# Optimization experiments

Hardware: AMD Instinct MI355X
Metric: run time of the kernel (lower is better)

## Reference

```python
import jax, jax.numpy as jnp
import numpy as np

NUM_STEPS = 50
NUM_DOF = 1
NVAR = NUM_STEPS * NUM_DOF
T = 0.05
V_MAX, A_MAX, J_MAX = 1.0, 2.0, 5.0
P_MAX = np.pi
THETA0 = 0.0
RHO = 1.0
MAXITER = 15
BATCH = 32768
HIDDEN = 1024
EPS = 1e-5


def _build_mats():
    # finite-difference operators (num_dof=1 so kron with eye(1) is identity)
    P_vel = np.eye(NUM_STEPS)
    P_acc = np.diff(P_vel, axis=0) / T          # (49, 50)
    P_jerk = np.diff(P_acc, axis=0) / T         # (48, 50)
    P_pos = np.cumsum(P_vel, axis=0) * T        # (50, 50)
    A_control = np.vstack([P_vel, -P_vel, P_acc, -P_acc,
                           P_jerk, -P_jerk, P_pos, -P_pos]).astype(np.float32)  # (394, 50)
    A_eq = np.zeros((2, NUM_STEPS), np.float32)
    A_eq[0, 0] = 1.0
    A_eq[1, -1] = 1.0
    cost = np.eye(NVAR) + RHO * A_control.T @ A_control
    Q = np.block([[cost, A_eq.T], [A_eq, np.zeros((2, 2))]])
    Q_inv = np.linalg.inv(Q).astype(np.float32)  # (52, 52)
    na = NUM_STEPS - 1
    nj = na - 1
    # limits used inside the iteration (p_max on both halves)
    b_iter = np.concatenate([np.full(2 * NUM_STEPS, V_MAX), np.full(2 * na, A_MAX),
                             np.full(2 * nj, J_MAX), np.full(2 * NUM_STEPS, P_MAX)]).astype(np.float32)
    # limits used for the slack init (p_max -/+ theta_init)
    b_init = np.concatenate([np.full(2 * NUM_STEPS, V_MAX), np.full(2 * na, A_MAX),
                             np.full(2 * nj, J_MAX), np.full(NUM_STEPS, P_MAX - THETA0),
                             np.full(NUM_STEPS, P_MAX + THETA0)]).astype(np.float32)
    return jnp.asarray(A_control), jnp.asarray(Q_inv), jnp.asarray(b_iter), jnp.asarray(b_init)


def _bn(x, g, b):
    # BatchNorm1d in training mode: biased batch statistics
    m = jnp.mean(x, axis=0)
    v = jnp.var(x, axis=0)
    return g * (x - m) * jax.lax.rsqrt(v + EPS) + b


def setup_inputs() -> dict:
    key = jax.random.key(0)
    ks = jax.random.split(key, 6)
    x = jax.random.normal(ks[0], (BATCH, NVAR), jnp.float32)
    W1 = jax.random.normal(ks[1], (NVAR, HIDDEN), jnp.float32) * 0.1
    W2 = jax.random.normal(ks[2], (HIDDEN, HIDDEN), jnp.float32) * 0.03
    W3 = jax.random.normal(ks[3], (HIDDEN, 256), jnp.float32) * 0.03
    W4 = jax.random.normal(ks[4], (256, 2 * NVAR), jnp.float32) * 0.06
    z = lambda n: jnp.zeros((n,), jnp.float32)
    o = lambda n: jnp.ones((n,), jnp.float32)
    return {"xi_samples_input_nn": x,
            "W1": W1, "b1": z(HIDDEN), "g1": o(HIDDEN), "be1": z(HIDDEN),
            "W2": W2, "b2": z(HIDDEN), "g2": o(HIDDEN), "be2": z(HIDDEN),
            "W3": W3, "b3": z(256), "g3": o(256), "be3": z(256),
            "W4": W4, "b4": z(2 * NVAR)}


def reference(xi_samples_input_nn, W1, b1, g1, be1, W2, b2, g2, be2,
              W3, b3, g3, be3, W4, b4):
    x = xi_samples_input_nn  # (B, nvar): both MLP input and projection target
    A_c, Q_inv, b_it, b_in = _build_mats()

    # MLP decoder
    h = jax.nn.relu(_bn(x @ W1 + b1, g1, be1))
    h = jax.nn.relu(_bn(h @ W2 + b2, g2, be2))
    h = jax.nn.relu(_bn(h @ W3 + b3, g3, be3))
    out = h @ W4 + b4                     # (B, 2*nvar)
    xi0 = out[:, :NVAR]
    lam0 = out[:, NVAR:2 * NVAR]

    s0 = jnp.maximum(0.0, b_in - xi0 @ A_c.T)        # (B, 394)
    b_eq = jnp.zeros((x.shape[0], 2), x.dtype)       # v_start = v_goal = 0

    def step(carry, _):
        xi, s, lam = carry
        b_aug = b_it - s
        # A_projection = I, so A_proj.T @ x.T -> x
        lincost = -lam - x - RHO * (b_aug @ A_c)
        rhs = jnp.concatenate([-lincost, b_eq], axis=1)   # (B, 52)
        sol = rhs @ Q_inv.T
        xi_n = sol[:, :NVAR]
        s_n = jnp.maximum(0.0, b_it - xi_n @ A_c.T)
        res = xi_n @ A_c.T - b_it + s_n
        res_norm = jnp.linalg.norm(res, axis=1)
        lam_n = lam - RHO * (res @ A_c)
        fp = (jnp.linalg.norm(xi - xi_n, axis=1)
              + jnp.linalg.norm(lam - lam_n, axis=1)
              + jnp.linalg.norm(s - s_n, axis=1))
        return (xi_n, s_n, lam_n), (res_norm, fp)

    (xi, s, lam), (primal, fixed_pt) = jax.lax.scan(step, (xi0, s0, lam0), None, length=MAXITER)
    avg_res_fixed_point = jnp.mean(fixed_pt, axis=0)  # (B,)
    avg_res_primal = jnp.mean(primal, axis=0)         # (B,)
    return xi, avg_res_fixed_point, avg_res_primal
```

## Files before the change

### kernel.cpp

```cpp
#include <hip/hip_runtime.h>
#include <math.h>

#define BATCH 32768
#define NVARS 50
#define H1 1024
#define H2 1024
#define H3 256
#define NOUT 100
#define EPSBN 1e-5f

#define TF   0.05f
#define AF   20.0f
#define JF   400.0f
#define VMAX 1.0f
#define AMAX 2.0f
#define JMAX 5.0f
#define PMAX 3.14159265358979323846f

typedef unsigned short ushort_t;
typedef __attribute__((ext_vector_type(8))) short short8;
typedef __attribute__((ext_vector_type(4))) float f32x4;
typedef __attribute__((ext_vector_type(2))) float f32x2;

__device__ float g_z1[(size_t)BATCH * H1];
__device__ float g_z2[(size_t)BATCH * H2];
__device__ float g_ps[32 * 1024];
__device__ float g_pq[32 * 1024];
__device__ float g_scale[3 * 1024];
__device__ float g_shift[3 * 1024];
__device__ float g_Mi[2500];
__device__ float g_xT[(size_t)NVARS * BATCH];
__device__ float g_nnT[(size_t)NOUT * BATCH];
__device__ ushort_t g_w2p[(size_t)3 * H1 * H2];
__device__ ushort_t g_w3p[(size_t)3 * H2 * H3];

__device__ __forceinline__ void split3(float f, ushort_t& h, ushort_t& m, ushort_t& l)
{
    unsigned u = __float_as_uint(f);
    unsigned r = u + 0x7fffu + ((u >> 16) & 1u);
    h = (ushort_t)(r >> 16);
    float f1 = f - __uint_as_float((unsigned)h << 16);
    unsigned u1 = __float_as_uint(f1);
    unsigned r1 = u1 + 0x7fffu + ((u1 >> 16) & 1u);
    m = (ushort_t)(r1 >> 16);
    float f2 = f1 - __uint_as_float((unsigned)m << 16);
    unsigned u2 = __float_as_uint(f2);
    unsigned r2 = u2 + 0x7fffu + ((u2 >> 16) & 1u);
    l = (ushort_t)(r2 >> 16);
}

__global__ void build_M(float* __restrict__ Mout)
{
    __shared__ double aug[52][104];
    __shared__ int piv;
    int tid = threadIdx.x;

    const double Tf = (double)0.05f;
    const double c3[3] = { 400.0, -800.0, 400.0 };

    for (int idx = tid; idx < 52 * 104; idx += 64) {
        int j = idx / 104, k = idx % 104;
        double v = 0.0;
        if (k >= 52) {
            v = (k == 52 + j) ? 1.0 : 0.0;
        } else if (j < 50 && k < 50) {
            double q = (j == k) ? 3.0 : 0.0;
            if (j == k) q += 800.0 * ((j < 49 ? 1 : 0) + (j > 0 ? 1 : 0));
            if (j - k == 1 || k - j == 1) q += -800.0;
            int lo = j > k ? j : k; lo -= 2; if (lo < 0) lo = 0;
            int hi = j < k ? j : k; if (hi > 47) hi = 47;
            for (int i = lo; i <= hi; ++i) {
                int dj = j - i, dk = k - i;
                if (dj >= 0 && dj <= 2 && dk >= 0 && dk <= 2)
                    q += 2.0 * c3[dj] * c3[dk];
            }
            int mx = j > k ? j : k;
            q += 2.0 * Tf * Tf * (double)(50 - mx);
            v = q;
        } else if ((j == 50 && k == 0) || (j == 0 && k == 50) ||
                   (j == 51 && k == 49) || (j == 49 && k == 51)) {
            v = 1.0;
        }
        aug[j][k] = v;
    }
    __syncthreads();

    for (int c = 0; c < 52; ++c) {
        if (tid == 0) {
            int p = c; double best = fabs(aug[c][c]);
            for (int r = c + 1; r < 52; ++r) {
                double v = fabs(aug[r][c]);
                if (v > best) { best = v; p = r; }
            }
            piv = p;
        }
        __syncthreads();
        int p = piv;
        if (p != c) {
            for (int k = tid; k < 104; k += 64) {
                double t = aug[c][k]; aug[c][k] = aug[p][k]; aug[p][k] = t;
            }
        }
        __syncthreads();
        double pv = aug[c][c];
        __syncthreads();
        for (int k = tid; k < 104; k += 64) aug[c][k] /= pv;
        __syncthreads();
        if (tid < 52 && tid != c) {
            double f = aug[tid][c];
            for (int k = 0; k < 104; ++k) aug[tid][k] -= f * aug[c][k];
        }
        __syncthreads();
    }

    for (int idx = tid; idx < 2500; idx += 64) {
        int k = idx / 50, j = idx % 50;
        Mout[idx] = (float)aug[j][52 + k];
    }
}

template <int C>
__global__ __launch_bounds__(64)
void transp(const float* __restrict__ Z, float* __restrict__ ZT)
{
    __shared__ float t[64][C + 1];
    const int lane = threadIdx.x;
    const size_t r0 = (size_t)blockIdx.x * 64;
#pragma unroll 1
    for (int i = 0; i < C; ++i) {
        int idx = i * 64 + lane;
        int r = idx / C, c = idx % C;
        t[r][c] = Z[r0 * C + idx];
    }
    __syncthreads();
#pragma unroll 1
    for (int c = 0; c < C; ++c)
        ZT[(size_t)c * BATCH + r0 + lane] = t[lane][c];
}

__global__ __launch_bounds__(512)
void wsplit_pack(const float* __restrict__ W, ushort_t* __restrict__ Wp,
                 int K, int N)
{
    int t = threadIdx.x;
    int n0 = blockIdx.x * 16, k0 = blockIdx.y * 32;
    int kk = t >> 4, nn = t & 15;
    float f = W[(size_t)(k0 + kk) * N + n0 + nn];
    ushort_t h, m, l;
    split3(f, h, m, l);
    int Nsub = N >> 4;
    int lane = (kk >> 3) * 16 + nn, e = kk & 7;
    size_t base = ((size_t)((k0 >> 5) * Nsub + (n0 >> 4)) * 3) * 512 + lane * 8 + e;
    Wp[base]        = h;
    Wp[base + 512]  = m;
    Wp[base + 1024] = l;
}

__global__ __launch_bounds__(256)
void gemm_mfma(const float* __restrict__ A, const ushort_t* __restrict__ Wp,
               const float* __restrict__ bias,
               const float* __restrict__ scale, const float* __restrict__ shift,
               float* __restrict__ C, int M, int K, int N, int ntn)
{
    __shared__ __attribute__((aligned(16))) ushort_t lds[3][4][64][8];

    const int nwg = gridDim.x;
    const int chunk = nwg >> 3;
    const int b = blockIdx.x;
    const int logical = (b & 7) * chunk + (b >> 3);
    const int rowt = logical / ntn;
    const int colt = logical - rowt * ntn;
    const int row0 = rowt * 64;
    const int col0s = colt * 16;

    const int t = threadIdx.x;
    const int lane = t & 63, wn = t >> 6;
    const int fr = lane & 15, fg = lane >> 4;
    const int srow = t & 63, skc = t >> 6;
    const int Nsub = N >> 4;

    f32x4 acc[4][4];
#pragma unroll
    for (int m = 0; m < 4; ++m)
#pragma unroll
        for (int n = 0; n < 4; ++n)
#pragma unroll
            for (int q = 0; q < 4; ++q) acc[m][n][q] = 0.f;

    int ks = 0;
    for (int k0 = 0; k0 < K; k0 += 32, ++ks) {
        {
            const float* ap = A + (size_t)(row0 + srow) * K + k0 + skc * 8;
            float4 f0 = *(const float4*)ap;
            float4 f1 = *(const float4*)(ap + 4);
            const float* scp = scale + k0 + skc * 8;
            const float* shp = shift + k0 + skc * 8;
            float4 sc0 = *(const float4*)scp, sc1 = *(const float4*)(scp + 4);
            float4 sh0 = *(const float4*)shp, sh1 = *(const float4*)(shp + 4);
            float v[8];
            v[0] = fmaxf(f0.x * sc0.x + sh0.x, 0.f);
            v[1] = fmaxf(f0.y * sc0.y + sh0.y, 0.f);
            v[2] = fmaxf(f0.z * sc0.z + sh0.z, 0.f);
            v[3] = fmaxf(f0.w * sc0.w + sh0.w, 0.f);
            v[4] = fmaxf(f1.x * sc1.x + sh1.x, 0.f);
            v[5] = fmaxf(f1.y * sc1.y + sh1.y, 0.f);
            v[6] = fmaxf(f1.z * sc1.z + sh1.z, 0.f);
            v[7] = fmaxf(f1.w * sc1.w + sh1.w, 0.f);
            ushort_t h_[8], m_[8], l_[8];
#pragma unroll
            for (int q = 0; q < 8; ++q) split3(v[q], h_[q], m_[q], l_[q]);
#define PK(a,b2) (((unsigned)(a)) | (((unsigned)(b2)) << 16))
            *(uint4*)&lds[0][skc][srow][0] = make_uint4(PK(h_[0],h_[1]), PK(h_[2],h_[3]), PK(h_[4],h_[5]), PK(h_[6],h_[7]));
            *(uint4*)&lds[1][skc][srow][0] = make_uint4(PK(m_[0],m_[1]), PK(m_[2],m_[3]), PK(m_[4],m_[5]), PK(m_[6],m_[7]));
            *(uint4*)&lds[2][skc][srow][0] = make_uint4(PK(l_[0],l_[1]), PK(l_[2],l_[3]), PK(l_[4],l_[5]), PK(l_[6],l_[7]));
#undef PK
        }
        __syncthreads();

        short8 b_h[4], b_m[4], b_l[4];
#pragma unroll
        for (int n = 0; n < 4; ++n) {
            size_t base = ((size_t)(ks * Nsub + col0s + wn * 4 + n) * 3) * 512 + lane * 8;
            b_h[n] = *(const short8*)(Wp + base);
            b_m[n] = *(const short8*)(Wp + base + 512);
            b_l[n] = *(const short8*)(Wp + base + 1024);
        }
#pragma unroll
        for (int m = 0; m < 4; ++m) {
            int r = m * 16 + fr;
            short8 a_h = *(const short8*)&lds[0][fg][r][0];
            short8 a_m = *(const short8*)&lds[1][fg][r][0];
            short8 a_l = *(const short8*)&lds[2][fg][r][0];
#pragma unroll
            for (int n = 0; n < 4; ++n) {
                f32x4 c = acc[m][n];
                c = __builtin_amdgcn_mfma_f32_16x16x32_bf16(a_l, b_h[n], c, 0, 0, 0);
                c = __builtin_amdgcn_mfma_f32_16x16x32_bf16(a_h, b_l[n], c, 0, 0, 0);
                c = __builtin_amdgcn_mfma_f32_16x16x32_bf16(a_m, b_m[n], c, 0, 0, 0);
                c = __builtin_amdgcn_mfma_f32_16x16x32_bf16(a_m, b_h[n], c, 0, 0, 0);
                c = __builtin_amdgcn_mfma_f32_16x16x32_bf16(a_h, b_m[n], c, 0, 0, 0);
                c = __builtin_amdgcn_mfma_f32_16x16x32_bf16(a_h, b_h[n], c, 0, 0, 0);
                acc[m][n] = c;
            }
        }
        __syncthreads();
    }

#pragma unroll
    for (int m = 0; m < 4; ++m)
#pragma unroll
        for (int n = 0; n < 4; ++n) {
            int cc = (col0s + wn * 4 + n) * 16 + fr;
            float bv = bias[cc];
#pragma unroll
            for (int q = 0; q < 4; ++q) {
                int rr = row0 + m * 16 + fg * 4 + q;
                C[(size_t)rr * N + cc] = acc[m][n][q] + bv;
            }
        }
}

template <int BN_APPLY>
__global__ __launch_bounds__(256)
void gemm_k(const float* __restrict__ A, const float* __restrict__ W,
            const float* __restrict__ bias,
            const float* __restrict__ scale, const float* __restrict__ shift,
            float* __restrict__ C, int M, int K, int N)
{
    const int BM = 128, BN = 128, BK = 16;
    __shared__ __attribute__((aligned(16))) float As[BK][BM + 4];
    __shared__ __attribute__((aligned(16))) float Ws[BK][BN];
    int tid = threadIdx.x;
    int tm = tid >> 4, tn = tid & 15;
    int row0 = blockIdx.x * BM, col0 = blockIdx.y * BN;

    float acc[8][8];
#pragma unroll
    for (int i = 0; i < 8; ++i)
#pragma unroll
        for (int j = 0; j < 8; ++j) acc[i][j] = 0.f;

    int alr = tid >> 4;
    int alk = tid & 15;
    int wlc = tid & 127;
    int wlk = tid >> 7;

    for (int k0 = 0; k0 < K; k0 += BK) {
#pragma unroll
        for (int i = 0; i < 8; ++i) {
            int rr = row0 + alr + i * 16;
            int kk = k0 + alk;
            float v = 0.f;
            if (kk < K) {
                v = A[(size_t)rr * K + kk];
                if (BN_APPLY) v = fmaxf(v * scale[kk] + shift[kk], 0.f);
            }
            As[alk][alr + i * 16] = v;
        }
#pragma unroll
        for (int i = 0; i < 8; ++i) {
            int kk = k0 + wlk + i * 2;
            int cc = col0 + wlc;
            Ws[wlk + i * 2][wlc] = (kk < K && cc < N) ? W[(size_t)kk * N + cc] : 0.f;
        }
        __syncthreads();
#pragma unroll
        for (int kk = 0; kk < BK; ++kk) {
            float av[8], wv[8];
            float4 tv;
            tv = *(const float4*)&As[kk][tm * 8];     av[0]=tv.x; av[1]=tv.y; av[2]=tv.z; av[3]=tv.w;
            tv = *(const float4*)&As[kk][tm * 8 + 4]; av[4]=tv.x; av[5]=tv.y; av[6]=tv.z; av[7]=tv.w;
            tv = *(const float4*)&Ws[kk][tn * 8];     wv[0]=tv.x; wv[1]=tv.y; wv[2]=tv.z; wv[3]=tv.w;
            tv = *(const float4*)&Ws[kk][tn * 8 + 4]; wv[4]=tv.x; wv[5]=tv.y; wv[6]=tv.z; wv[7]=tv.w;
#pragma unroll
            for (int i = 0; i < 8; ++i)
#pragma unroll
                for (int j = 0; j < 8; ++j) acc[i][j] += av[i] * wv[j];
        }
        __syncthreads();
    }
#pragma unroll
    for (int i = 0; i < 8; ++i) {
        int rr = row0 + tm * 8 + i;
#pragma unroll
        for (int j = 0; j < 8; ++j) {
            int cc = col0 + tn * 8 + j;
            if (cc < N) C[(size_t)rr * N + cc] = acc[i][j] + bias[cc];
        }
    }
}

__global__ __launch_bounds__(256)
void stats_part(const float* __restrict__ Z, float* __restrict__ ps,
                float* __restrict__ pq, int M, int C, int chunks)
{
    int lc = threadIdx.x & 63;
    int col = blockIdx.x * 64 + lc;
    int rg = threadIdx.x >> 6;
    int rpc = M / chunks;
    int r0 = blockIdx.y * rpc;
    float s = 0.f, q = 0.f;
    for (int rr = r0 + rg; rr < r0 + rpc; rr += 4) {
        float v = Z[(size_t)rr * C + col];
        s += v; q += v * v;
    }
    __shared__ float ls[4][64], lq[4][64];
    ls[rg][lc] = s; lq[rg][lc] = q;
    __syncthreads();
    if (rg == 0) {
        float S = ls[0][lc] + ls[1][lc] + ls[2][lc] + ls[3][lc];
        float Q = lq[0][lc] + lq[1][lc] + lq[2][lc] + lq[3][lc];
        ps[(size_t)blockIdx.y * C + col] = S;
        pq[(size_t)blockIdx.y * C + col] = Q;
    }
}

__global__ void stats_fin(const float* __restrict__ ps, const float* __restrict__ pq,
                          const float* __restrict__ g, const float* __restrict__ be,
                          float* __restrict__ scale, float* __restrict__ shift,
                          int C, int M, int chunks)
{
    int c = blockIdx.x * blockDim.x + threadIdx.x;
    if (c >= C) return;
    float S = 0.f, Q = 0.f;
    for (int i = 0; i < chunks; ++i) { S += ps[(size_t)i * C + c]; Q += pq[(size_t)i * C + c]; }
    float inv = 1.0f / (float)M;
    float mean = S * inv;
    float var = Q * inv - mean * mean;
    float rstd = 1.0f / sqrtf(var + EPSBN);
    float sc = g[c] * rstd;
    scale[c] = sc;
    shift[c] = be[c] - mean * sc;
}

__global__ __launch_bounds__(64, 1)
void iter_k(const float* __restrict__ XT, const float* __restrict__ NNT,
            const float* __restrict__ MiT, float* __restrict__ out)
{
    __shared__ float sA[50 * 64];
    __shared__ float sB[50 * 64];
    __shared__ float sLam[50 * 64];
    __shared__ float sXv[50 * 64];
    const int lane = threadIdx.x;
    const int row = blockIdx.x * 64 + lane;
#define IDX(k) (((k) << 6) + lane)

#pragma unroll 1
    for (int k = 0; k < 50; ++k) {
        sA[IDX(k)]   = NNT[(size_t)k * BATCH + row];
        sLam[IDX(k)] = NNT[(size_t)(50 + k) * BATCH + row];
        sXv[IDX(k)]  = XT[(size_t)k * BATCH + row];
    }
    float* cx = sA;
    float* cn = sB;
    float fps = 0.f, prs = 0.f;
    float rh[50];

#pragma unroll 1
    for (int it = 0; it < 15; ++it) {
#pragma unroll
        for (int k = 0; k < 50; ++k) rh[k] = 0.f;
        {
            float pre = 0.f, Sp = 0.f, ap = 0.f;
            float xc = cx[IDX(0)];
#pragma unroll
            for (int k = 0; k < 50; ++k) {
                float xn = (k < 49) ? cx[IDX(k + 1)] : 0.f;
                rh[k] += fminf(VMAX, xc) - fminf(VMAX, -xc);
                rh[k] -= TF * Sp;
                pre += xc;
                float p = TF * pre;
                Sp += fminf(PMAX, p) - fminf(PMAX, -p);
                if (k < 49) {
                    float a = AF * (xn - xc);
                    float da = fminf(AMAX, a) - fminf(AMAX, -a);
                    rh[k] -= AF * da; rh[k + 1] += AF * da;
                    if (k >= 1) {
                        float j = AF * (a - ap);
                        float dj = fminf(JMAX, j) - fminf(JMAX, -j);
                        rh[k - 1] += JF * dj; rh[k] -= 2.f * JF * dj; rh[k + 1] += JF * dj;
                    }
                    ap = a;
                }
                xc = xn;
            }
            float Stot = TF * Sp;
#pragma unroll
            for (int k = 0; k < 50; ++k)
                rh[k] = rh[k] + sLam[IDX(k)] + sXv[IDX(k)] + Stot;
        }

        {
            f32x2 xr[25];
#pragma unroll
            for (int j = 0; j < 25; ++j) { xr[j].x = 0.f; xr[j].y = 0.f; }
#pragma unroll
            for (int k = 0; k < 50; ++k) {
                f32x2 rv2; rv2.x = rh[k]; rv2.y = rh[k];
                const f32x2* Mrow = (const f32x2*)(MiT + k * 50);
#pragma unroll
                for (int j = 0; j < 25; ++j) xr[j] += Mrow[j] * rv2;
            }
#pragma unroll
            for (int j = 0; j < 25; ++j) {
                cn[IDX(2 * j)]     = xr[j].x;
                cn[IDX(2 * j + 1)] = xr[j].y;
            }
        }

        float res2 = 0.f, ds2 = 0.f, dxi2 = 0.f, dlam2 = 0.f;
#pragma unroll
        for (int k = 0; k < 50; ++k) rh[k] = 0.f;
        {
            float preo = 0.f, pren = 0.f, SpF = 0.f, aop = 0.f, anp = 0.f;
            float xoc = cx[IDX(0)], xnc = cn[IDX(0)];
#pragma unroll
            for (int k = 0; k < 50; ++k) {
                float xon = (k < 49) ? cx[IDX(k + 1)] : 0.f;
                float xnn = (k < 49) ? cn[IDX(k + 1)] : 0.f;
                float d = xoc - xnc; dxi2 += d * d;
                float rp = fmaxf(xnc - VMAX, 0.f), rm = fmaxf(-xnc - VMAX, 0.f);
                res2 += rp * rp + rm * rm;
                float so = fmaxf(VMAX - xoc, 0.f), sn = fmaxf(VMAX - xnc, 0.f);
                d = so - sn; ds2 += d * d;
                so = fmaxf(VMAX + xoc, 0.f); sn = fmaxf(VMAX + xnc, 0.f);
                d = so - sn; ds2 += d * d;
                rh[k] += rp - rm;
                rh[k] -= TF * SpF;
                preo += xoc; pren += xnc;
                float po = TF * preo, pn = TF * pren;
                rp = fmaxf(pn - PMAX, 0.f); rm = fmaxf(-pn - PMAX, 0.f);
                res2 += rp * rp + rm * rm;
                so = fmaxf(PMAX - po, 0.f); sn = fmaxf(PMAX - pn, 0.f);
                d = so - sn; ds2 += d * d;
                so = fmaxf(PMAX + po, 0.f); sn = fmaxf(PMAX + pn, 0.f);
                d = so - sn; ds2 += d * d;
                SpF += rp - rm;
                if (k < 49) {
                    float ao = AF * (xon - xoc), an = AF * (xnn - xnc);
                    rp = fmaxf(an - AMAX, 0.f); rm = fmaxf(-an - AMAX, 0.f);
                    res2 += rp * rp + rm * rm;
                    so = fmaxf(AMAX - ao, 0.f); sn = fmaxf(AMAX - an, 0.f);
                    d = so - sn; ds2 += d * d;
                    so = fmaxf(AMAX + ao, 0.f); sn = fmaxf(AMAX + an, 0.f);
                    d = so - sn; ds2 += d * d;
                    float fa = rp - rm; rh[k] -= AF * fa; rh[k + 1] += AF * fa;
                    if (k >= 1) {
                        float jo = AF * (ao - aop), jn = AF * (an - anp);
                        rp = fmaxf(jn - JMAX, 0.f); rm = fmaxf(-jn - JMAX, 0.f);
                        res2 += rp * rp + rm * rm;
                        so = fmaxf(JMAX - jo, 0.f); sn = fmaxf(JMAX - jn, 0.f);
                        d = so - sn; ds2 += d * d;
                        so = fmaxf(JMAX + jo, 0.f); sn = fmaxf(JMAX + jn, 0.f);
                        d = so - sn; ds2 += d * d;
                        float fj = rp - rm;
                        rh[k - 1] += JF * fj; rh[k] -= 2.f * JF * fj; rh[k + 1] += JF * fj;
                    }
                    aop = ao; anp = an;
                }
                xoc = xon; xnc = xnn;
            }
            float SF = TF * SpF;
#pragma unroll
            for (int k = 0; k < 50; ++k) {
                float gk = rh[k] + SF;
                dlam2 += gk * gk;
                sLam[IDX(k)] -= gk;
            }
        }
        prs += sqrtf(res2);
        fps += sqrtf(dxi2) + sqrtf(dlam2) + sqrtf(ds2);
        float* tp = cx; cx = cn; cn = tp;
    }
#pragma unroll 1
    for (int k = 0; k < 50; ++k) out[(size_t)row * 50 + k] = cx[IDX(k)];
    out[(size_t)BATCH * 50 + row] = fps * (1.f / 15.f);
    out[(size_t)BATCH * 51 + row] = prs * (1.f / 15.f);
#undef IDX
}

extern "C" void kernel_launch(void* const* d_in, const int* in_sizes, int n_in,
                              void* d_out, int out_size, void* d_ws, size_t ws_size,
                              hipStream_t stream)
{
    const float* x   = (const float*)d_in[0];
    const float* W1  = (const float*)d_in[1];
    const float* b1  = (const float*)d_in[2];
    const float* g1  = (const float*)d_in[3];
    const float* be1 = (const float*)d_in[4];
    const float* W2  = (const float*)d_in[5];
    const float* b2  = (const float*)d_in[6];
    const float* g2  = (const float*)d_in[7];
    const float* be2 = (const float*)d_in[8];
    const float* W3  = (const float*)d_in[9];
    const float* b3  = (const float*)d_in[10];
    const float* g3  = (const float*)d_in[11];
    const float* be3 = (const float*)d_in[12];
    const float* W4  = (const float*)d_in[13];
    const float* b4  = (const float*)d_in[14];

    float *z1, *z2, *ps, *pq, *scb, *shb, *Mi, *xT, *nnT;
    ushort_t *w2p, *w3p;
    hipGetSymbolAddress((void**)&z1,  HIP_SYMBOL(g_z1));
    hipGetSymbolAddress((void**)&z2,  HIP_SYMBOL(g_z2));
    hipGetSymbolAddress((void**)&ps,  HIP_SYMBOL(g_ps));
    hipGetSymbolAddress((void**)&pq,  HIP_SYMBOL(g_pq));
    hipGetSymbolAddress((void**)&scb, HIP_SYMBOL(g_scale));
    hipGetSymbolAddress((void**)&shb, HIP_SYMBOL(g_shift));
    hipGetSymbolAddress((void**)&Mi,  HIP_SYMBOL(g_Mi));
    hipGetSymbolAddress((void**)&xT,  HIP_SYMBOL(g_xT));
    hipGetSymbolAddress((void**)&nnT, HIP_SYMBOL(g_nnT));
    hipGetSymbolAddress((void**)&w2p, HIP_SYMBOL(g_w2p));
    hipGetSymbolAddress((void**)&w3p, HIP_SYMBOL(g_w3p));

    float* z3  = z1;
    float* nno = z1 + (size_t)BATCH * H3;
    float* sc1 = scb;        float* sh1 = shb;
    float* sc2 = scb + 1024; float* sh2 = shb + 1024;
    float* sc3 = scb + 2048; float* sh3 = shb + 2048;

    dim3 blk(256);
    hipLaunchKernelGGL(build_M, dim3(1), dim3(64), 0, stream, Mi);
    hipLaunchKernelGGL(wsplit_pack, dim3(H2 / 16, H1 / 32), dim3(512), 0, stream, W2, w2p, H1, H2);
    hipLaunchKernelGGL(wsplit_pack, dim3(H3 / 16, H2 / 32), dim3(512), 0, stream, W3, w3p, H2, H3);
    hipLaunchKernelGGL((transp<50>), dim3(BATCH / 64), dim3(64), 0, stream, x, xT);

    hipLaunchKernelGGL((gemm_k<0>), dim3(BATCH / 128, H1 / 128), blk, 0, stream,
                       x, W1, b1, (const float*)nullptr, (const float*)nullptr,
                       z1, BATCH, NVARS, H1);
    hipLaunchKernelGGL(stats_part, dim3(H1 / 64, 32), blk, 0, stream, z1, ps, pq, BATCH, H1, 32);
    hipLaunchKernelGGL(stats_fin, dim3(4), dim3(256), 0, stream, ps, pq, g1, be1, sc1, sh1, H1, BATCH, 32);
    hipLaunchKernelGGL(gemm_mfma, dim3((BATCH / 64) * (H2 / 256)), blk, 0, stream,
                       z1, w2p, b2, sc1, sh1, z2, BATCH, H1, H2, H2 / 256);
    hipLaunchKernelGGL(stats_part, dim3(H2 / 64, 32), blk, 0, stream, z2, ps, pq, BATCH, H2, 32);
    hipLaunchKernelGGL(stats_fin, dim3(4), dim3(256), 0, stream, ps, pq, g2, be2, sc2, sh2, H2, BATCH, 32);
    hipLaunchKernelGGL(gemm_mfma, dim3((BATCH / 64) * (H3 / 256)), blk, 0, stream,
                       z2, w3p, b3, sc2, sh2, z3, BATCH, H2, H3, H3 / 256);
    hipLaunchKernelGGL(stats_part, dim3(H3 / 64, 32), blk, 0, stream, z3, ps, pq, BATCH, H3, 32);
    hipLaunchKernelGGL(stats_fin, dim3(1), dim3(256), 0, stream, ps, pq, g3, be3, sc3, sh3, H3, BATCH, 32);
    hipLaunchKernelGGL((gemm_k<1>), dim3(BATCH / 128, 1), blk, 0, stream,
                       z3, W4, b4, sc3, sh3, nno, BATCH, H3, NOUT);
    hipLaunchKernelGGL((transp<100>), dim3(BATCH / 64), dim3(64), 0, stream, nno, nnT);
    hipLaunchKernelGGL(iter_k, dim3(BATCH / 64), dim3(64), 0, stream,
                       xT, nnT, Mi, (float*)d_out);
}
```

Measured before the change: 1.778 ms.

## Split each ADMM row across two lanes for the 50x50 solve matvec

The iteration kernel now assigns two lanes per batch row, with each lane computing half of the 50x50 matrix-vector product against a padded, parity-split copy of the inverse matrix read as float4. The right-hand side is staged through a new shared buffer so both lanes can read it, and the grid doubles to twice as many blocks of 32 rows. The intent is to halve the per-thread matvec work and register pressure and to raise occupancy. The cost is that the constraint-projection and residual passes are now computed redundantly by both lanes of a row, and the kernel does extra shared-memory traffic.

```diff
diff --git a/kernel.cpp b/kernel.cpp
--- a/kernel.cpp
+++ b/kernel.cpp
@@ -20,7 +20,6 @@
 typedef unsigned short ushort_t;
 typedef __attribute__((ext_vector_type(8))) short short8;
 typedef __attribute__((ext_vector_type(4))) float f32x4;
-typedef __attribute__((ext_vector_type(2))) float f32x2;
 
 __device__ float g_z1[(size_t)BATCH * H1];
 __device__ float g_z2[(size_t)BATCH * H2];
@@ -28,7 +27,7 @@
 __device__ float g_pq[32 * 1024];
 __device__ float g_scale[3 * 1024];
 __device__ float g_shift[3 * 1024];
-__device__ float g_Mi[2500];
+__device__ float g_Mp[2800];
 __device__ float g_xT[(size_t)NVARS * BATCH];
 __device__ float g_nnT[(size_t)NOUT * BATCH];
 __device__ ushort_t g_w2p[(size_t)3 * H1 * H2];
@@ -113,9 +112,12 @@
         __syncthreads();
     }
 
-    for (int idx = tid; idx < 2500; idx += 64) {
-        int k = idx / 50, j = idx % 50;
-        Mout[idx] = (float)aug[j][52 + k];
+    for (int idx = tid; idx < 2800; idx += 64) {
+        int slot = idx % 28;
+        int kk2 = idx / 28;
+        int k = kk2 >> 1, par = kk2 & 1;
+        int j = par * 25 + slot;
+        Mout[idx] = (slot < 25) ? (float)aug[j][52 + k] : 0.f;
     }
 }
 
@@ -375,26 +377,31 @@
 
 __global__ __launch_bounds__(64, 1)
 void iter_k(const float* __restrict__ XT, const float* __restrict__ NNT,
-            const float* __restrict__ MiT, float* __restrict__ out)
-{
-    __shared__ float sA[50 * 64];
-    __shared__ float sB[50 * 64];
-    __shared__ float sLam[50 * 64];
-    __shared__ float sXv[50 * 64];
+            const float* __restrict__ Mp, float* __restrict__ out)
+{
+    __shared__ float sA[50 * 32];
+    __shared__ float sB[50 * 32];
+    __shared__ float sLam[50 * 32];
+    __shared__ float sXv[50 * 32];
+    __shared__ float sRh[50 * 32];
     const int lane = threadIdx.x;
-    const int row = blockIdx.x * 64 + lane;
-#define IDX(k) (((k) << 6) + lane)
+    const int r = lane >> 1, par = lane & 1;
+    const int base = blockIdx.x * 32;
+    const int row = base + r;
+#define IDX2(k) (((k) << 5) + r)
 
 #pragma unroll 1
-    for (int k = 0; k < 50; ++k) {
-        sA[IDX(k)]   = NNT[(size_t)k * BATCH + row];
-        sLam[IDX(k)] = NNT[(size_t)(50 + k) * BATCH + row];
-        sXv[IDX(k)]  = XT[(size_t)k * BATCH + row];
+    for (int idx = lane; idx < 1600; idx += 64) {
+        int k = idx >> 5, rr = idx & 31;
+        sA[idx]   = NNT[(size_t)k * BATCH + base + rr];
+        sLam[idx] = NNT[(size_t)(50 + k) * BATCH + base + rr];
+        sXv[idx]  = XT[(size_t)k * BATCH + base + rr];
     }
     float* cx = sA;
     float* cn = sB;
     float fps = 0.f, prs = 0.f;
     float rh[50];
+    const float* mp = Mp + par * 28;
 
 #pragma unroll 1
     for (int it = 0; it < 15; ++it) {
@@ -402,10 +409,10 @@
         for (int k = 0; k < 50; ++k) rh[k] = 0.f;
         {
             float pre = 0.f, Sp = 0.f, ap = 0.f;
-            float xc = cx[IDX(0)];
+            float xc = cx[IDX2(0)];
 #pragma unroll
             for (int k = 0; k < 50; ++k) {
-                float xn = (k < 49) ? cx[IDX(k + 1)] : 0.f;
+                float xn = (k < 49) ? cx[IDX2(k + 1)] : 0.f;
                 rh[k] += fminf(VMAX, xc) - fminf(VMAX, -xc);
                 rh[k] -= TF * Sp;
                 pre += xc;
@@ -427,25 +434,29 @@
             float Stot = TF * Sp;
 #pragma unroll
             for (int k = 0; k < 50; ++k)
-                rh[k] = rh[k] + sLam[IDX(k)] + sXv[IDX(k)] + Stot;
+                sRh[IDX2(k)] = rh[k] + sLam[IDX2(k)] + sXv[IDX2(k)] + Stot;
         }
 
         {
-            f32x2 xr[25];
-#pragma unroll
-            for (int j = 0; j < 25; ++j) { xr[j].x = 0.f; xr[j].y = 0.f; }
-#pragma unroll
+            float xr[28];
+#pragma unroll
+            for (int jj = 0; jj < 28; ++jj) xr[jj] = 0.f;
+#pragma unroll 2
             for (int k = 0; k < 50; ++k) {
-                f32x2 rv2; rv2.x = rh[k]; rv2.y = rh[k];
-                const f32x2* Mrow = (const f32x2*)(MiT + k * 50);
-#pragma unroll
-                for (int j = 0; j < 25; ++j) xr[j] += Mrow[j] * rv2;
-            }
-#pragma unroll
-            for (int j = 0; j < 25; ++j) {
-                cn[IDX(2 * j)]     = xr[j].x;
-                cn[IDX(2 * j + 1)] = xr[j].y;
-            }
+                float rv = sRh[IDX2(k)];
+                const float4* m4 = (const float4*)(mp + k * 56);
+#pragma unroll
+                for (int q = 0; q < 7; ++q) {
+                    float4 mv = m4[q];
+                    xr[q * 4 + 0] += mv.x * rv;
+                    xr[q * 4 + 1] += mv.y * rv;
+                    xr[q * 4 + 2] += mv.z * rv;
+                    xr[q * 4 + 3] += mv.w * rv;
+                }
+            }
+#pragma unroll
+            for (int jj = 0; jj < 25; ++jj)
+                cn[((par * 25 + jj) << 5) + r] = xr[jj];
         }
 
         float res2 = 0.f, ds2 = 0.f, dxi2 = 0.f, dlam2 = 0.f;
@@ -453,11 +464,11 @@
         for (int k = 0; k < 50; ++k) rh[k] = 0.f;
         {
             float preo = 0.f, pren = 0.f, SpF = 0.f, aop = 0.f, anp = 0.f;
-            float xoc = cx[IDX(0)], xnc = cn[IDX(0)];
+            float xoc = cx[IDX2(0)], xnc = cn[IDX2(0)];
 #pragma unroll
             for (int k = 0; k < 50; ++k) {
-                float xon = (k < 49) ? cx[IDX(k + 1)] : 0.f;
-                float xnn = (k < 49) ? cn[IDX(k + 1)] : 0.f;
+                float xon = (k < 49) ? cx[IDX2(k + 1)] : 0.f;
+                float xnn = (k < 49) ? cn[IDX2(k + 1)] : 0.f;
                 float d = xoc - xnc; dxi2 += d * d;
                 float rp = fmaxf(xnc - VMAX, 0.f), rm = fmaxf(-xnc - VMAX, 0.f);
                 res2 += rp * rp + rm * rm;
@@ -505,7 +516,7 @@
             for (int k = 0; k < 50; ++k) {
                 float gk = rh[k] + SF;
                 dlam2 += gk * gk;
-                sLam[IDX(k)] -= gk;
+                sLam[IDX2(k)] -= gk;
             }
         }
         prs += sqrtf(res2);
@@ -513,10 +524,13 @@
         float* tp = cx; cx = cn; cn = tp;
     }
 #pragma unroll 1
-    for (int k = 0; k < 50; ++k) out[(size_t)row * 50 + k] = cx[IDX(k)];
+    for (int idx = lane; idx < 1600; idx += 64) {
+        int rr = idx / 50, kk = idx - rr * 50;
+        out[(size_t)(base + rr) * 50 + kk] = cx[(kk << 5) + rr];
+    }
     out[(size_t)BATCH * 50 + row] = fps * (1.f / 15.f);
     out[(size_t)BATCH * 51 + row] = prs * (1.f / 15.f);
-#undef IDX
+#undef IDX2
 }
 
 extern "C" void kernel_launch(void* const* d_in, const int* in_sizes, int n_in,
@@ -539,7 +553,7 @@
     const float* W4  = (const float*)d_in[13];
     const float* b4  = (const float*)d_in[14];
 
-    float *z1, *z2, *ps, *pq, *scb, *shb, *Mi, *xT, *nnT;
+    float *z1, *z2, *ps, *pq, *scb, *shb, *Mp, *xT, *nnT;
     ushort_t *w2p, *w3p;
     hipGetSymbolAddress((void**)&z1,  HIP_SYMBOL(g_z1));
     hipGetSymbolAddress((void**)&z2,  HIP_SYMBOL(g_z2));
@@ -547,7 +561,7 @@
     hipGetSymbolAddress((void**)&pq,  HIP_SYMBOL(g_pq));
     hipGetSymbolAddress((void**)&scb, HIP_SYMBOL(g_scale));
     hipGetSymbolAddress((void**)&shb, HIP_SYMBOL(g_shift));
-    hipGetSymbolAddress((void**)&Mi,  HIP_SYMBOL(g_Mi));
+    hipGetSymbolAddress((void**)&Mp,  HIP_SYMBOL(g_Mp));
     hipGetSymbolAddress((void**)&xT,  HIP_SYMBOL(g_xT));
     hipGetSymbolAddress((void**)&nnT, HIP_SYMBOL(g_nnT));
     hipGetSymbolAddress((void**)&w2p, HIP_SYMBOL(g_w2p));
@@ -560,7 +574,7 @@
     float* sc3 = scb + 2048; float* sh3 = shb + 2048;
 
     dim3 blk(256);
-    hipLaunchKernelGGL(build_M, dim3(1), dim3(64), 0, stream, Mi);
+    hipLaunchKernelGGL(build_M, dim3(1), dim3(64), 0, stream, Mp);
     hipLaunchKernelGGL(wsplit_pack, dim3(H2 / 16, H1 / 32), dim3(512), 0, stream, W2, w2p, H1, H2);
     hipLaunchKernelGGL(wsplit_pack, dim3(H3 / 16, H2 / 32), dim3(512), 0, stream, W3, w3p, H2, H3);
     hipLaunchKernelGGL((transp<50>), dim3(BATCH / 64), dim3(64), 0, stream, x, xT);
@@ -581,6 +595,6 @@
     hipLaunchKernelGGL((gemm_k<1>), dim3(BATCH / 128, 1), blk, 0, stream,
                        z3, W4, b4, sc3, sh3, nno, BATCH, H3, NOUT);
     hipLaunchKernelGGL((transp<100>), dim3(BATCH / 64), dim3(64), 0, stream, nno, nnT);
-    hipLaunchKernelGGL(iter_k, dim3(BATCH / 64), dim3(64), 0, stream,
-                       xT, nnT, Mi, (float*)d_out);
-}
+    hipLaunchKernelGGL(iter_k, dim3(BATCH / 32), dim3(64), 0, stream,
+                       xT, nnT, Mp, (float*)d_out);
+}
```

After: 1.758 ms. Within noise of the previous version (-1.1%).
